# Kernel tuning notes

Measured on AMD Instinct MI355X. Metric: run time of the kernel, lower is better.

The kernel has to match this reference:

```python
import math
import jax, jax.numpy as jnp
import numpy as np

N_HEADS, INPUT_DIM, EMBED_DIM = 8, 512, 512
KEY_DIM = EMBED_DIM // N_HEADS  # 64, val_dim == key_dim
BATCH, N = 4, 2048


def setup_inputs() -> dict:
    key = jax.random.key(0)
    ks = jax.random.split(key, 6)
    def unif(k, shape):
        stdv = 1.0 / math.sqrt(shape[-1])
        return jax.random.uniform(k, shape, jnp.float32, -stdv, stdv)
    q = jax.random.normal(ks[0], (BATCH, N, INPUT_DIM), jnp.float32)
    mask = jax.random.randint(ks[1], (BATCH, N, N), 0, 2, jnp.int32)
    W_query = unif(ks[2], (N_HEADS, INPUT_DIM, KEY_DIM))
    W_key = unif(ks[3], (N_HEADS, INPUT_DIM, KEY_DIM))
    W_val = unif(ks[4], (N_HEADS, INPUT_DIM, KEY_DIM))
    W_out = unif(ks[5], (N_HEADS, KEY_DIM, EMBED_DIM))
    return {"q": q, "mask": mask, "W_query": W_query, "W_key": W_key,
            "W_val": W_val, "W_out": W_out}


def reference(q, mask, W_query, W_key, W_val, W_out):
    # Self-attention: k is None, v is None -> k = q, v = q (module forward_).
    norm = 1.0 / math.sqrt(KEY_DIM)
    m = mask.astype(bool)[None]  # (1, b, nq, ng) broadcast over heads
    Q = jnp.einsum('bnd,hdk->hbnk', q, W_query)  # (h, b, nq, dk)
    K = jnp.einsum('bnd,hdk->hbnk', q, W_key)    # (h, b, ng, dk)
    V = jnp.einsum('bnd,hdv->hbnv', q, W_val)    # (h, b, ng, dv)
    scores = norm * jnp.einsum('hbqk,hbgk->hbqg', Q, K)  # (h, b, nq, ng)
    scores = jnp.where(m, -jnp.inf, scores)
    attn = jax.nn.softmax(scores, axis=-1)
    attn = jnp.where(m, 0.0, attn)  # zero out masked (also kills NaN rows)
    heads = jnp.einsum('hbqg,hbgv->hbqv', attn, V)
    out = jnp.einsum('hbqv,hve->bqe', heads, W_out)  # (b, nq, embed)
    return out
```

## Files before the change

kernel.cpp:

```cpp
#include <hip/hip_runtime.h>
#include <hip/hip_bf16.h>
#include <stdint.h>

using bf16 = __hip_bfloat16;
typedef __attribute__((ext_vector_type(8))) short short8;
typedef __attribute__((ext_vector_type(4))) short short4b;
typedef __attribute__((ext_vector_type(4))) float f32x4;
typedef __attribute__((ext_vector_type(4))) unsigned int u32x4;

#if __has_builtin(__builtin_amdgcn_exp2f)
#define EXP2(x) __builtin_amdgcn_exp2f(x)
#else
#define EXP2(x) exp2f(x)
#endif

__device__ __forceinline__ short8 load8(const bf16* p) {
  return *reinterpret_cast<const short8*>(p);
}
__device__ __forceinline__ short4b load4(const bf16* p) {
  return *reinterpret_cast<const short4b*>(p);
}
__device__ __forceinline__ short f2b(float f) {
  return __builtin_bit_cast(short, __float2bfloat16(f));
}
__device__ __forceinline__ unsigned int pk2(float a, float b) {
  return (unsigned int)(unsigned short)f2b(a) |
         ((unsigned int)(unsigned short)f2b(b) << 16);
}
__device__ __forceinline__ void asy16(const bf16* g, bf16* l) {
  __builtin_amdgcn_global_load_lds(
      (const __attribute__((address_space(1))) void*)g,
      (__attribute__((address_space(3))) void*)l, 16, 0, 0);
}

__global__ void k_prep(const float4* __restrict__ x, ushort4* __restrict__ xb,
                       const float* __restrict__ Wq, const float* __restrict__ Wk,
                       const float* __restrict__ Wv, const float* __restrict__ Wo,
                       bf16* __restrict__ Wcat, bf16* __restrict__ Wot,
                       const int4* __restrict__ m4,
                       unsigned long long* __restrict__ bits) {
  int blk = blockIdx.x;
  if (blk < 4096) {
    int i = blk * 256 + threadIdx.x;
    float4 v = x[i];
    ushort4 o;
    o.x = (unsigned short)f2b(v.x);
    o.y = (unsigned short)f2b(v.y);
    o.z = (unsigned short)f2b(v.z);
    o.w = (unsigned short)f2b(v.w);
    xb[i] = o;
  } else if (blk < 8192) {
    int t = (blk - 4096) * 256 + threadIdx.x;
    if (t < 786432) {
      int rr = t >> 9, d = t & 511;
      int which = rr >> 9;
      int hdk = rr & 511, h = hdk >> 6, dk = hdk & 63;
      const float* W = (which == 0) ? Wq : ((which == 1) ? Wk : Wv);
      float v = W[(h * 512 + d) * 64 + dk];
      if (which == 0) v *= 0.18033688011112042f;
      Wcat[t] = __float2bfloat16(v);
    } else {
      int u = t - 786432;
      int e = u >> 9, hv = u & 511;
      Wot[u] = __float2bfloat16(Wo[hv * 512 + e]);
    }
  } else {
    int i = (blk - 8192) * 256 + threadIdx.x;
    int4 v = m4[i];
    unsigned int nib = (unsigned)(v.x != 0) | ((unsigned)(v.y != 0) << 1) |
                       ((unsigned)(v.z != 0) << 2) | ((unsigned)(v.w != 0) << 3);
    unsigned long long w = (unsigned long long)nib << (4 * (threadIdx.x & 15));
    w |= __shfl_xor(w, 1);
    w |= __shfl_xor(w, 2);
    w |= __shfl_xor(w, 4);
    w |= __shfl_xor(w, 8);
    if ((threadIdx.x & 15) == 0) bits[i >> 4] = w;
  }
}

__device__ __forceinline__ void gemm128(const bf16* __restrict__ A,
                                        const bf16* __restrict__ Bt,
                                        bf16* As, bf16* Bs,
                                        int rowBase, int colBase,
                                        f32x4 acc[4][4]) {
  const int tid = threadIdx.x;
  const int lane = tid & 63, w = tid >> 6;
  const int g = lane >> 4, r = lane & 15;

  auto stage = [&](int buf, int s) {
#pragma unroll
    for (int p = 0; p < 4; ++p) {
      int c = p * 256 + tid;
      int row = c >> 3, w8 = c & 7, sg = w8 ^ (row & 7);
      asy16(A + (size_t)(rowBase + row) * 512 + s * 64 + sg * 8,
            As + buf * 8192 + c * 8);
    }
#pragma unroll
    for (int p = 0; p < 4; ++p) {
      int c = p * 256 + tid;
      int row = c >> 3, w8 = c & 7, sg = w8 ^ (row & 7);
      asy16(Bt + (size_t)(colBase + row) * 512 + s * 64 + sg * 8,
            Bs + buf * 8192 + c * 8);
    }
  };

  stage(0, 0);
  int buf = 0;
  const int rbl = (w >> 1) * 64, cbl = (w & 1) * 64;
  for (int s = 0; s < 8; ++s) {
    __syncthreads();
    if (s < 7) stage(buf ^ 1, s + 1);
    const bf16* a0 = As + buf * 8192;
    const bf16* b0 = Bs + buf * 8192;
#pragma unroll
    for (int kk = 0; kk < 2; ++kk) {
      short8 af[4], bfr[4];
#pragma unroll
      for (int mt = 0; mt < 4; ++mt) {
        int row = rbl + mt * 16 + r;
        af[mt] = load8(a0 + (row * 8 + ((kk * 4 + g) ^ (row & 7))) * 8);
      }
#pragma unroll
      for (int nt = 0; nt < 4; ++nt) {
        int col = cbl + nt * 16 + r;
        bfr[nt] = load8(b0 + (col * 8 + ((kk * 4 + g) ^ (col & 7))) * 8);
      }
#pragma unroll
      for (int mt = 0; mt < 4; ++mt)
#pragma unroll
        for (int nt = 0; nt < 4; ++nt)
          acc[mt][nt] = __builtin_amdgcn_mfma_f32_16x16x32_bf16(
              af[mt], bfr[nt], acc[mt][nt], 0, 0, 0);
    }
    buf ^= 1;
  }
}

__global__ __launch_bounds__(256, 2) void k_proj_qkv(
    const bf16* __restrict__ Xb, const bf16* __restrict__ Wcat,
    bf16* __restrict__ Qb, bf16* __restrict__ Kb, bf16* __restrict__ Vt) {
  __shared__ __align__(16) bf16 As[2 * 8192];
  __shared__ __align__(16) bf16 Bs[2 * 8192];
  int rowBase = blockIdx.x * 128, colBase = blockIdx.y * 128;
  f32x4 acc[4][4] = {};
  gemm128(Xb, Wcat, As, Bs, rowBase, colBase, acc);
  const int lane = threadIdx.x & 63, w = threadIdx.x >> 6;
  const int g = lane >> 4, r = lane & 15;
#pragma unroll
  for (int mt = 0; mt < 4; ++mt) {
    int row0 = rowBase + (w >> 1) * 64 + mt * 16 + 4 * g;
    int b = row0 >> 11, n0 = row0 & 2047;
#pragma unroll
    for (int nt = 0; nt < 4; ++nt) {
      int col = colBase + (w & 1) * 64 + nt * 16 + r;
      if (col < 1024) {
        bf16* dst = (col < 512) ? Qb : Kb;
        int hh = (col >> 6) & 7, dk = col & 63;
        bf16* p0 = dst + ((size_t)(b * 8 + hh) * 2048 + n0) * 64 + dk;
#pragma unroll
        for (int rr = 0; rr < 4; ++rr)
          p0[rr * 64] = __float2bfloat16(acc[mt][nt][rr]);
      } else {
        int hdv = col - 1024;
        short4b pkv;
#pragma unroll
        for (int rr = 0; rr < 4; ++rr) pkv[rr] = f2b(acc[mt][nt][rr]);
        *reinterpret_cast<short4b*>(Vt + ((size_t)b * 512 + hdv) * 2048 + n0) = pkv;
      }
    }
  }
}

__global__ __launch_bounds__(256, 2) void k_proj_out(
    const bf16* __restrict__ O, const bf16* __restrict__ Wot,
    float* __restrict__ out) {
  __shared__ __align__(16) bf16 As[2 * 8192];
  __shared__ __align__(16) bf16 Bs[2 * 8192];
  int rowBase = blockIdx.x * 128, colBase = blockIdx.y * 128;
  f32x4 acc[4][4] = {};
  gemm128(O, Wot, As, Bs, rowBase, colBase, acc);
  const int lane = threadIdx.x & 63, w = threadIdx.x >> 6;
  const int g = lane >> 4, r = lane & 15;
#pragma unroll
  for (int mt = 0; mt < 4; ++mt) {
    int row0 = rowBase + (w >> 1) * 64 + mt * 16 + 4 * g;
#pragma unroll
    for (int nt = 0; nt < 4; ++nt) {
      int col = colBase + (w & 1) * 64 + nt * 16 + r;
#pragma unroll
      for (int rr = 0; rr < 4; ++rr)
        out[(size_t)(row0 + rr) * 512 + col] = acc[mt][nt][rr];
    }
  }
}

__global__ __launch_bounds__(256, 2) void k_attn(const bf16* __restrict__ Q,
    const bf16* __restrict__ K, const bf16* __restrict__ Vt,
    const unsigned long long* __restrict__ MB, bf16* __restrict__ O) {
  const int blin = blockIdx.x;
  const int j = blin >> 3;
  const int bh = (blin & 7) * 4 + (j >> 4);
  const int qt = j & 15;
  const int b = bh >> 3, h = bh & 7;
  const int tid = threadIdx.x;
  const int lane = tid & 63;
  const int wave = tid >> 6;
  const int g = lane >> 4, r = lane & 15;
  const int rx = r & 7;
  const int qbase = qt * 128 + wave * 32;

  __shared__ __align__(16) bf16 Kl[3][64 * 64];
  __shared__ __align__(16) bf16 Vl[3][64 * 64];

  const bf16* Kp = K + (size_t)bh * 2048 * 64;
  const bf16* Vp = Vt + (size_t)bh * 64 * 2048;

  short8 qf[2][2];
#pragma unroll
  for (int s = 0; s < 2; ++s) {
    const bf16* Qp = Q + ((size_t)bh * 2048 + qbase + s * 16 + r) * 64;
    qf[s][0] = load8(Qp + g * 8);
    qf[s][1] = load8(Qp + 32 + g * 8);
  }
  const unsigned long long* Mp0 = MB + ((size_t)b * 2048 + qbase + r) * 32;
  const unsigned long long* Mp1 = MB + ((size_t)b * 2048 + qbase + 16 + r) * 32;

  short8 ones;
#pragma unroll
  for (int i = 0; i < 8; ++i) ones[i] = (short)0x3F80;

  f32x4 acc[2][4] = {};
  f32x4 acc_l[2] = {};

  auto stage = [&](int buf, int kt) {
    const bf16* Kg = Kp + kt * 4096;
    const bf16* Vg = Vp + kt * 64;
#pragma unroll
    for (int p = 0; p < 2; ++p) {
      int c = p * 256 + tid;
      int row = c >> 3, gr = c & 7, sg = gr ^ (row & 7);
      asy16(Kg + row * 64 + sg * 8, &Kl[buf][0] + c * 8);
    }
#pragma unroll
    for (int p = 0; p < 2; ++p) {
      int c = p * 256 + tid;
      int row = c >> 3, gr = c & 7, sg = gr ^ (row & 7);
      asy16(Vg + (size_t)row * 2048 + sg * 8, &Vl[buf][0] + c * 8);
    }
  };

  auto qk = [&](const bf16* kl, f32x4 stl[4][2]) {
#pragma unroll
    for (int kc = 0; kc < 4; ++kc) {
      const bf16* krow = kl + (kc * 16 + r) * 64;
      short8 kf0 = load8(krow + ((g) ^ rx) * 8);
      short8 kf1 = load8(krow + ((4 + g) ^ rx) * 8);
      f32x4 z0 = {};
      z0 = __builtin_amdgcn_mfma_f32_16x16x32_bf16(kf0, qf[0][0], z0, 0, 0, 0);
      stl[kc][0] = __builtin_amdgcn_mfma_f32_16x16x32_bf16(kf1, qf[0][1], z0, 0, 0, 0);
      f32x4 z1 = {};
      z1 = __builtin_amdgcn_mfma_f32_16x16x32_bf16(kf0, qf[1][0], z1, 0, 0, 0);
      stl[kc][1] = __builtin_amdgcn_mfma_f32_16x16x32_bf16(kf1, qf[1][1], z1, 0, 0, 0);
    }
  };

  stage(0, 0);
  stage(1, 1);
  unsigned long long mw0c = Mp0[0], mw1c = Mp1[0];
  __syncthreads();
  f32x4 st_cur[4][2];
  qk(&Kl[0][0], st_cur);

  int b_cur = 0, b_nxt = 1, b_st = 2;

  for (int kt = 0; kt < 32; ++kt) {
    __syncthreads();
    if (kt < 30) stage(b_st, kt + 2);
    unsigned long long mw0n = 0, mw1n = 0;
    if (kt < 31) { mw0n = Mp0[kt + 1]; mw1n = Mp1[kt + 1]; }

    f32x4 stn[4][2];
    if (kt < 31) qk(&Kl[b_nxt][0], stn);

    short8 pa[2][2];
#pragma unroll
    for (int s = 0; s < 2; ++s) {
      unsigned long long mw = s ? mw1c : mw0c;
      unsigned ml = (unsigned)mw >> (4 * g);
      unsigned mh = (unsigned)(mw >> 32) >> (4 * g);
      float p[16];
#pragma unroll
      for (int kc = 0; kc < 4; ++kc)
#pragma unroll
        for (int rr = 0; rr < 4; ++rr) {
          float e = EXP2(st_cur[kc][s][rr]);
          unsigned wsel = (kc & 2) ? mh : ml;
          bool bad = (wsel >> (((kc & 1) << 4) + rr)) & 1u;
          p[kc * 4 + rr] = bad ? 0.f : e;
        }
      u32x4 q0, q1;
#pragma unroll
      for (int i2 = 0; i2 < 4; ++i2) {
        q0[i2] = pk2(p[2 * i2], p[2 * i2 + 1]);
        q1[i2] = pk2(p[8 + 2 * i2], p[8 + 2 * i2 + 1]);
      }
      pa[s][0] = __builtin_bit_cast(short8, q0);
      pa[s][1] = __builtin_bit_cast(short8, q1);
      acc_l[s] = __builtin_amdgcn_mfma_f32_16x16x32_bf16(pa[s][0], ones, acc_l[s], 0, 0, 0);
      acc_l[s] = __builtin_amdgcn_mfma_f32_16x16x32_bf16(pa[s][1], ones, acc_l[s], 0, 0, 0);
    }

    const bf16* vl = &Vl[b_cur][0];
#pragma unroll
    for (int dvs = 0; dvs < 4; ++dvs) {
      const bf16* vrow = vl + (dvs * 16 + r) * 64 + (g & 1) * 4;
      short4b v0 = load4(vrow + (((g >> 1)) ^ rx) * 8);
      short4b v1 = load4(vrow + ((2 + (g >> 1)) ^ rx) * 8);
      short4b v2 = load4(vrow + ((4 + (g >> 1)) ^ rx) * 8);
      short4b v3 = load4(vrow + ((6 + (g >> 1)) ^ rx) * 8);
      short8 vb0 = {v0[0], v0[1], v0[2], v0[3], v1[0], v1[1], v1[2], v1[3]};
      short8 vb1 = {v2[0], v2[1], v2[2], v2[3], v3[0], v3[1], v3[2], v3[3]};
#pragma unroll
      for (int s = 0; s < 2; ++s) {
        acc[s][dvs] = __builtin_amdgcn_mfma_f32_16x16x32_bf16(pa[s][0], vb0, acc[s][dvs], 0, 0, 0);
        acc[s][dvs] = __builtin_amdgcn_mfma_f32_16x16x32_bf16(pa[s][1], vb1, acc[s][dvs], 0, 0, 0);
      }
    }

#pragma unroll
    for (int kc = 0; kc < 4; ++kc) {
      st_cur[kc][0] = stn[kc][0];
      st_cur[kc][1] = stn[kc][1];
    }
    mw0c = mw0n;
    mw1c = mw1n;
    int t = b_cur; b_cur = b_nxt; b_nxt = b_st; b_st = t;
  }

#pragma unroll
  for (int s = 0; s < 2; ++s) {
    float inv[4];
#pragma unroll
    for (int rr = 0; rr < 4; ++rr)
      inv[rr] = (acc_l[s][rr] > 0.f) ? 1.f / acc_l[s][rr] : 0.f;
    bf16* Op = O + ((size_t)b * 2048 + qbase + s * 16 + 4 * g) * 512 + h * 64;
#pragma unroll
    for (int dvs = 0; dvs < 4; ++dvs)
#pragma unroll
      for (int rr = 0; rr < 4; ++rr)
        Op[rr * 512 + dvs * 16 + r] = __float2bfloat16(acc[s][dvs][rr] * inv[rr]);
  }
}


extern "C" void kernel_launch(void* const* d_in, const int* in_sizes, int n_in,
                              void* d_out, int out_size, void* d_ws, size_t ws_size,
                              hipStream_t stream) {
  const float* q    = (const float*)d_in[0];
  const int*   mask = (const int*)d_in[1];
  const float* Wq   = (const float*)d_in[2];
  const float* Wk   = (const float*)d_in[3];
  const float* Wv   = (const float*)d_in[4];
  const float* Wo   = (const float*)d_in[5];
  float* out = (float*)d_out;

  char* ws = (char*)d_ws;
  const size_t MB1 = 1024 * 1024;
  bf16* Xb   = (bf16*)(ws + 0);
  bf16* Qb   = (bf16*)(ws + 8 * MB1);
  bf16* Kb   = (bf16*)(ws + 16 * MB1);
  bf16* Vtb  = (bf16*)(ws + 24 * MB1);
  bf16* Ob   = (bf16*)(ws + 32 * MB1);
  unsigned long long* Mbits = (unsigned long long*)(ws + 40 * MB1);
  bf16* Wcat = (bf16*)(ws + 42 * MB1);
  bf16* Wot  = (bf16*)(ws + 42 * MB1 + 1536 * 512 * 2);

  k_prep<<<24576, 256, 0, stream>>>((const float4*)q, (ushort4*)Xb,
                                    Wq, Wk, Wv, Wo, Wcat, Wot,
                                    (const int4*)mask, Mbits);
  k_proj_qkv<<<dim3(64, 12), 256, 0, stream>>>(Xb, Wcat, Qb, Kb, Vtb);
  k_attn<<<512, 256, 0, stream>>>(Qb, Kb, Vtb, Mbits, Ob);
  k_proj_out<<<dim3(64, 4), 256, 0, stream>>>(Ob, Wot, out);
}
```

Before: 216.7 us.

## Pre-swizzle K/V into MFMA fragment layout and tile weight transposes

The QKV projection epilogue now writes K and V directly in per-64-key-tile, fragment-ordered layouts. This lets the attention kernel stage them with contiguous async copies and read each MFMA operand with a single 16-byte LDS load, replacing swizzled row loads and the four 8-byte V loads. The weight transpose in the prep kernel is rewritten as a 64x64 shared-memory tiled transpose with vectorized loads and stores instead of strided scalar gathers. The GEMM K-step is halved to 32 to cut LDS use, and the QKV kernel's launch bounds are raised to 3 blocks per CU. The risks are scattered 2-byte K stores in the projection epilogue and more barriers per GEMM.

```diff
diff --git a/kernel.cpp b/kernel.cpp
--- a/kernel.cpp
+++ b/kernel.cpp
@@ -17,9 +17,6 @@
 __device__ __forceinline__ short8 load8(const bf16* p) {
   return *reinterpret_cast<const short8*>(p);
 }
-__device__ __forceinline__ short4b load4(const bf16* p) {
-  return *reinterpret_cast<const short4b*>(p);
-}
 __device__ __forceinline__ short f2b(float f) {
   return __builtin_bit_cast(short, __float2bfloat16(f));
 }
@@ -32,6 +29,7 @@
       (const __attribute__((address_space(1))) void*)g,
       (__attribute__((address_space(3))) void*)l, 16, 0, 0);
 }
+
 
 __global__ void k_prep(const float4* __restrict__ x, ushort4* __restrict__ xb,
                        const float* __restrict__ Wq, const float* __restrict__ Wk,
@@ -40,8 +38,9 @@
                        const int4* __restrict__ m4,
                        unsigned long long* __restrict__ bits) {
   int blk = blockIdx.x;
+  const int tid = threadIdx.x;
   if (blk < 4096) {
-    int i = blk * 256 + threadIdx.x;
+    int i = blk * 256 + tid;
     float4 v = x[i];
     ushort4 o;
     o.x = (unsigned short)f2b(v.x);
@@ -49,32 +48,68 @@
     o.z = (unsigned short)f2b(v.z);
     o.w = (unsigned short)f2b(v.w);
     xb[i] = o;
-  } else if (blk < 8192) {
-    int t = (blk - 4096) * 256 + threadIdx.x;
-    if (t < 786432) {
-      int rr = t >> 9, d = t & 511;
-      int which = rr >> 9;
-      int hdk = rr & 511, h = hdk >> 6, dk = hdk & 63;
+  } else if (blk < 4352) {
+    int t = blk - 4096;
+    __shared__ float T[64][65];
+    if (t < 192) {
+      int which = t >> 6;
+      int h = (t >> 3) & 7, dt = t & 7;
       const float* W = (which == 0) ? Wq : ((which == 1) ? Wk : Wv);
-      float v = W[(h * 512 + d) * 64 + dk];
-      if (which == 0) v *= 0.18033688011112042f;
-      Wcat[t] = __float2bfloat16(v);
+#pragma unroll
+      for (int p = 0; p < 4; ++p) {
+        int row = p * 16 + (tid >> 4);
+        float4 v = *(const float4*)(W + (size_t)(h * 512 + dt * 64 + row) * 64 +
+                                    (tid & 15) * 4);
+        T[row][(tid & 15) * 4 + 0] = v.x;
+        T[row][(tid & 15) * 4 + 1] = v.y;
+        T[row][(tid & 15) * 4 + 2] = v.z;
+        T[row][(tid & 15) * 4 + 3] = v.w;
+      }
+      __syncthreads();
+      float scale = (which == 0) ? 0.18033688011112042f : 1.0f;
+      int jj = tid >> 2, i0 = (tid & 3) * 16;
+#pragma unroll
+      for (int q = 0; q < 2; ++q) {
+        short8 o;
+#pragma unroll
+        for (int e = 0; e < 8; ++e) o[e] = f2b(T[i0 + q * 8 + e][jj] * scale);
+        *(short8*)(Wcat + (size_t)(which * 512 + h * 64 + jj) * 512 + dt * 64 +
+                   i0 + q * 8) = o;
+      }
     } else {
-      int u = t - 786432;
-      int e = u >> 9, hv = u & 511;
-      Wot[u] = __float2bfloat16(Wo[hv * 512 + e]);
+      int t2 = t - 192;
+      int h = t2 >> 3, et = t2 & 7;
+#pragma unroll
+      for (int p = 0; p < 4; ++p) {
+        int row = p * 16 + (tid >> 4);
+        float4 v = *(const float4*)(Wo + (size_t)(h * 64 + row) * 512 + et * 64 +
+                                    (tid & 15) * 4);
+        T[row][(tid & 15) * 4 + 0] = v.x;
+        T[row][(tid & 15) * 4 + 1] = v.y;
+        T[row][(tid & 15) * 4 + 2] = v.z;
+        T[row][(tid & 15) * 4 + 3] = v.w;
+      }
+      __syncthreads();
+      int jj = tid >> 2, i0 = (tid & 3) * 16;
+#pragma unroll
+      for (int q = 0; q < 2; ++q) {
+        short8 o;
+#pragma unroll
+        for (int e = 0; e < 8; ++e) o[e] = f2b(T[i0 + q * 8 + e][jj]);
+        *(short8*)(Wot + (size_t)(et * 64 + jj) * 512 + h * 64 + i0 + q * 8) = o;
+      }
     }
   } else {
-    int i = (blk - 8192) * 256 + threadIdx.x;
+    int i = (blk - 4352) * 256 + tid;
     int4 v = m4[i];
     unsigned int nib = (unsigned)(v.x != 0) | ((unsigned)(v.y != 0) << 1) |
                        ((unsigned)(v.z != 0) << 2) | ((unsigned)(v.w != 0) << 3);
-    unsigned long long w = (unsigned long long)nib << (4 * (threadIdx.x & 15));
+    unsigned long long w = (unsigned long long)nib << (4 * (tid & 15));
     w |= __shfl_xor(w, 1);
     w |= __shfl_xor(w, 2);
     w |= __shfl_xor(w, 4);
     w |= __shfl_xor(w, 8);
-    if ((threadIdx.x & 15) == 0) bits[i >> 4] = w;
+    if ((tid & 15) == 0) bits[i >> 4] = w;
   }
 }
 
@@ -89,58 +124,55 @@
 
   auto stage = [&](int buf, int s) {
 #pragma unroll
-    for (int p = 0; p < 4; ++p) {
+    for (int p = 0; p < 2; ++p) {
       int c = p * 256 + tid;
-      int row = c >> 3, w8 = c & 7, sg = w8 ^ (row & 7);
-      asy16(A + (size_t)(rowBase + row) * 512 + s * 64 + sg * 8,
-            As + buf * 8192 + c * 8);
-    }
-#pragma unroll
-    for (int p = 0; p < 4; ++p) {
+      int row = c >> 2, gr = c & 3, sg = gr ^ (row & 3);
+      asy16(A + (size_t)(rowBase + row) * 512 + s * 32 + sg * 8,
+            As + buf * 4096 + c * 8);
+    }
+#pragma unroll
+    for (int p = 0; p < 2; ++p) {
       int c = p * 256 + tid;
-      int row = c >> 3, w8 = c & 7, sg = w8 ^ (row & 7);
-      asy16(Bt + (size_t)(colBase + row) * 512 + s * 64 + sg * 8,
-            Bs + buf * 8192 + c * 8);
+      int row = c >> 2, gr = c & 3, sg = gr ^ (row & 3);
+      asy16(Bt + (size_t)(colBase + row) * 512 + s * 32 + sg * 8,
+            Bs + buf * 4096 + c * 8);
     }
   };
 
   stage(0, 0);
   int buf = 0;
   const int rbl = (w >> 1) * 64, cbl = (w & 1) * 64;
-  for (int s = 0; s < 8; ++s) {
+  for (int s = 0; s < 16; ++s) {
     __syncthreads();
-    if (s < 7) stage(buf ^ 1, s + 1);
-    const bf16* a0 = As + buf * 8192;
-    const bf16* b0 = Bs + buf * 8192;
-#pragma unroll
-    for (int kk = 0; kk < 2; ++kk) {
-      short8 af[4], bfr[4];
-#pragma unroll
-      for (int mt = 0; mt < 4; ++mt) {
-        int row = rbl + mt * 16 + r;
-        af[mt] = load8(a0 + (row * 8 + ((kk * 4 + g) ^ (row & 7))) * 8);
-      }
-#pragma unroll
-      for (int nt = 0; nt < 4; ++nt) {
-        int col = cbl + nt * 16 + r;
-        bfr[nt] = load8(b0 + (col * 8 + ((kk * 4 + g) ^ (col & 7))) * 8);
-      }
-#pragma unroll
-      for (int mt = 0; mt < 4; ++mt)
-#pragma unroll
-        for (int nt = 0; nt < 4; ++nt)
-          acc[mt][nt] = __builtin_amdgcn_mfma_f32_16x16x32_bf16(
-              af[mt], bfr[nt], acc[mt][nt], 0, 0, 0);
-    }
+    if (s < 15) stage(buf ^ 1, s + 1);
+    const bf16* a0 = As + buf * 4096;
+    const bf16* b0 = Bs + buf * 4096;
+    short8 af[4], bfr[4];
+#pragma unroll
+    for (int mt = 0; mt < 4; ++mt) {
+      int row = rbl + mt * 16 + r;
+      af[mt] = load8(a0 + (row * 4 + (g ^ (row & 3))) * 8);
+    }
+#pragma unroll
+    for (int nt = 0; nt < 4; ++nt) {
+      int col = cbl + nt * 16 + r;
+      bfr[nt] = load8(b0 + (col * 4 + (g ^ (col & 3))) * 8);
+    }
+#pragma unroll
+    for (int mt = 0; mt < 4; ++mt)
+#pragma unroll
+      for (int nt = 0; nt < 4; ++nt)
+        acc[mt][nt] = __builtin_amdgcn_mfma_f32_16x16x32_bf16(
+            af[mt], bfr[nt], acc[mt][nt], 0, 0, 0);
     buf ^= 1;
   }
 }
 
-__global__ __launch_bounds__(256, 2) void k_proj_qkv(
+__global__ __launch_bounds__(256, 3) void k_proj_qkv(
     const bf16* __restrict__ Xb, const bf16* __restrict__ Wcat,
-    bf16* __restrict__ Qb, bf16* __restrict__ Kb, bf16* __restrict__ Vt) {
-  __shared__ __align__(16) bf16 As[2 * 8192];
-  __shared__ __align__(16) bf16 Bs[2 * 8192];
+    bf16* __restrict__ Qb, bf16* __restrict__ Kp, bf16* __restrict__ Vp) {
+  __shared__ __align__(16) bf16 As[2 * 4096];
+  __shared__ __align__(16) bf16 Bs[2 * 4096];
   int rowBase = blockIdx.x * 128, colBase = blockIdx.y * 128;
   f32x4 acc[4][4] = {};
   gemm128(Xb, Wcat, As, Bs, rowBase, colBase, acc);
@@ -150,22 +182,39 @@
   for (int mt = 0; mt < 4; ++mt) {
     int row0 = rowBase + (w >> 1) * 64 + mt * 16 + 4 * g;
     int b = row0 >> 11, n0 = row0 & 2047;
+    int kt = n0 >> 6;
 #pragma unroll
     for (int nt = 0; nt < 4; ++nt) {
       int col = colBase + (w & 1) * 64 + nt * 16 + r;
-      if (col < 1024) {
-        bf16* dst = (col < 512) ? Qb : Kb;
-        int hh = (col >> 6) & 7, dk = col & 63;
-        bf16* p0 = dst + ((size_t)(b * 8 + hh) * 2048 + n0) * 64 + dk;
+      if (col < 512) {
+        int hh = col >> 6, dk = col & 63;
+        bf16* p0 = Qb + ((size_t)(b * 8 + hh) * 2048 + n0) * 64 + dk;
 #pragma unroll
         for (int rr = 0; rr < 4; ++rr)
           p0[rr * 64] = __float2bfloat16(acc[mt][nt][rr]);
+      } else if (col < 1024) {
+        int hh = (col >> 6) & 7, dk = col & 63;
+        int half = dk >> 5, gk = (dk >> 3) & 3, jj = dk & 7;
+        int kr = n0 & 63;
+        int kc = kr >> 4, r0 = kr & 15;
+        bf16* base = Kp + (size_t)(b * 8 + hh) * 131072 + (size_t)kt * 4096 +
+                     ((kc * 2 + half) * 4 + gk) * 128 + jj;
+#pragma unroll
+        for (int rr = 0; rr < 4; ++rr)
+          base[(r0 + rr) * 8] = __float2bfloat16(acc[mt][nt][rr]);
       } else {
         int hdv = col - 1024;
+        int hh = hdv >> 6, dv = hdv & 63;
+        int dvs = dv >> 4, rv = dv & 15;
+        int kcol0 = n0 & 63;
+        int half = kcol0 >> 5, gv = (kcol0 >> 2) & 3;
+        int j0 = ((kcol0 >> 4) & 1) * 4;
         short4b pkv;
 #pragma unroll
         for (int rr = 0; rr < 4; ++rr) pkv[rr] = f2b(acc[mt][nt][rr]);
-        *reinterpret_cast<short4b*>(Vt + ((size_t)b * 512 + hdv) * 2048 + n0) = pkv;
+        *reinterpret_cast<short4b*>(
+            Vp + (size_t)(b * 8 + hh) * 131072 + (size_t)kt * 4096 +
+            (((half * 4 + dvs) * 4 + gv) * 16 + rv) * 8 + j0) = pkv;
       }
     }
   }
@@ -174,8 +223,8 @@
 __global__ __launch_bounds__(256, 2) void k_proj_out(
     const bf16* __restrict__ O, const bf16* __restrict__ Wot,
     float* __restrict__ out) {
-  __shared__ __align__(16) bf16 As[2 * 8192];
-  __shared__ __align__(16) bf16 Bs[2 * 8192];
+  __shared__ __align__(16) bf16 As[2 * 4096];
+  __shared__ __align__(16) bf16 Bs[2 * 4096];
   int rowBase = blockIdx.x * 128, colBase = blockIdx.y * 128;
   f32x4 acc[4][4] = {};
   gemm128(O, Wot, As, Bs, rowBase, colBase, acc);
@@ -195,7 +244,7 @@
 }
 
 __global__ __launch_bounds__(256, 2) void k_attn(const bf16* __restrict__ Q,
-    const bf16* __restrict__ K, const bf16* __restrict__ Vt,
+    const bf16* __restrict__ K, const bf16* __restrict__ V,
     const unsigned long long* __restrict__ MB, bf16* __restrict__ O) {
   const int blin = blockIdx.x;
   const int j = blin >> 3;
@@ -206,14 +255,13 @@
   const int lane = tid & 63;
   const int wave = tid >> 6;
   const int g = lane >> 4, r = lane & 15;
-  const int rx = r & 7;
   const int qbase = qt * 128 + wave * 32;
 
-  __shared__ __align__(16) bf16 Kl[3][64 * 64];
-  __shared__ __align__(16) bf16 Vl[3][64 * 64];
-
-  const bf16* Kp = K + (size_t)bh * 2048 * 64;
-  const bf16* Vp = Vt + (size_t)bh * 64 * 2048;
+  __shared__ __align__(16) bf16 Kl[3][4096];
+  __shared__ __align__(16) bf16 Vl[3][4096];
+
+  const bf16* Kp = K + (size_t)bh * 131072;
+  const bf16* Vp = V + (size_t)bh * 131072;
 
   short8 qf[2][2];
 #pragma unroll
@@ -233,28 +281,25 @@
   f32x4 acc_l[2] = {};
 
   auto stage = [&](int buf, int kt) {
-    const bf16* Kg = Kp + kt * 4096;
-    const bf16* Vg = Vp + kt * 64;
+    const bf16* Kg = Kp + (size_t)kt * 4096;
+    const bf16* Vg = Vp + (size_t)kt * 4096;
 #pragma unroll
     for (int p = 0; p < 2; ++p) {
       int c = p * 256 + tid;
-      int row = c >> 3, gr = c & 7, sg = gr ^ (row & 7);
-      asy16(Kg + row * 64 + sg * 8, &Kl[buf][0] + c * 8);
+      asy16(Kg + c * 8, &Kl[buf][0] + c * 8);
     }
 #pragma unroll
     for (int p = 0; p < 2; ++p) {
       int c = p * 256 + tid;
-      int row = c >> 3, gr = c & 7, sg = gr ^ (row & 7);
-      asy16(Vg + (size_t)row * 2048 + sg * 8, &Vl[buf][0] + c * 8);
+      asy16(Vg + c * 8, &Vl[buf][0] + c * 8);
     }
   };
 
   auto qk = [&](const bf16* kl, f32x4 stl[4][2]) {
 #pragma unroll
     for (int kc = 0; kc < 4; ++kc) {
-      const bf16* krow = kl + (kc * 16 + r) * 64;
-      short8 kf0 = load8(krow + ((g) ^ rx) * 8);
-      short8 kf1 = load8(krow + ((4 + g) ^ rx) * 8);
+      short8 kf0 = load8(kl + ((kc * 2 + 0) * 4 + g) * 128 + r * 8);
+      short8 kf1 = load8(kl + ((kc * 2 + 1) * 4 + g) * 128 + r * 8);
       f32x4 z0 = {};
       z0 = __builtin_amdgcn_mfma_f32_16x16x32_bf16(kf0, qf[0][0], z0, 0, 0, 0);
       stl[kc][0] = __builtin_amdgcn_mfma_f32_16x16x32_bf16(kf1, qf[0][1], z0, 0, 0, 0);
@@ -313,13 +358,8 @@
     const bf16* vl = &Vl[b_cur][0];
 #pragma unroll
     for (int dvs = 0; dvs < 4; ++dvs) {
-      const bf16* vrow = vl + (dvs * 16 + r) * 64 + (g & 1) * 4;
-      short4b v0 = load4(vrow + (((g >> 1)) ^ rx) * 8);
-      short4b v1 = load4(vrow + ((2 + (g >> 1)) ^ rx) * 8);
-      short4b v2 = load4(vrow + ((4 + (g >> 1)) ^ rx) * 8);
-      short4b v3 = load4(vrow + ((6 + (g >> 1)) ^ rx) * 8);
-      short8 vb0 = {v0[0], v0[1], v0[2], v0[3], v1[0], v1[1], v1[2], v1[3]};
-      short8 vb1 = {v2[0], v2[1], v2[2], v2[3], v3[0], v3[1], v3[2], v3[3]};
+      short8 vb0 = load8(vl + ((0 * 4 + dvs) * 4 + g) * 128 + r * 8);
+      short8 vb1 = load8(vl + ((1 * 4 + dvs) * 4 + g) * 128 + r * 8);
 #pragma unroll
       for (int s = 0; s < 2; ++s) {
         acc[s][dvs] = __builtin_amdgcn_mfma_f32_16x16x32_bf16(pa[s][0], vb0, acc[s][dvs], 0, 0, 0);
@@ -368,17 +408,17 @@
   const size_t MB1 = 1024 * 1024;
   bf16* Xb   = (bf16*)(ws + 0);
   bf16* Qb   = (bf16*)(ws + 8 * MB1);
-  bf16* Kb   = (bf16*)(ws + 16 * MB1);
-  bf16* Vtb  = (bf16*)(ws + 24 * MB1);
+  bf16* Kpm  = (bf16*)(ws + 16 * MB1);
+  bf16* Vpm  = (bf16*)(ws + 24 * MB1);
   bf16* Ob   = (bf16*)(ws + 32 * MB1);
   unsigned long long* Mbits = (unsigned long long*)(ws + 40 * MB1);
   bf16* Wcat = (bf16*)(ws + 42 * MB1);
   bf16* Wot  = (bf16*)(ws + 42 * MB1 + 1536 * 512 * 2);
 
-  k_prep<<<24576, 256, 0, stream>>>((const float4*)q, (ushort4*)Xb,
+  k_prep<<<20736, 256, 0, stream>>>((const float4*)q, (ushort4*)Xb,
                                     Wq, Wk, Wv, Wo, Wcat, Wot,
                                     (const int4*)mask, Mbits);
-  k_proj_qkv<<<dim3(64, 12), 256, 0, stream>>>(Xb, Wcat, Qb, Kb, Vtb);
-  k_attn<<<512, 256, 0, stream>>>(Qb, Kb, Vtb, Mbits, Ob);
+  k_proj_qkv<<<dim3(64, 12), 256, 0, stream>>>(Xb, Wcat, Qb, Kpm, Vpm);
+  k_attn<<<512, 256, 0, stream>>>(Qb, Kpm, Vpm, Mbits, Ob);
   k_proj_out<<<dim3(64, 4), 256, 0, stream>>>(Ob, Wot, out);
 }
```

New measurement: 214.2 us. About the same (-1.1%).
